# Performance work log

Hardware: AMD Instinct MI355X
Metric: run time of the kernel (lower is better)

## Reference

```python
import jax, jax.numpy as jnp
import numpy as np
from math import sqrt

BLOCK = 64  # block_size from init_kwargs


def setup_inputs() -> dict:
    key = jax.random.key(0)
    kq, kk, kv = jax.random.split(key, 3)
    b, t, e = 16, 8192, 64
    return {
        "Q": jax.random.normal(kq, (b, t, e), dtype=jnp.float32),
        "K": jax.random.normal(kk, (b, t, e), dtype=jnp.float32),
        "V": jax.random.normal(kv, (b, t, e), dtype=jnp.float32),
    }


def reference(Q, K, V):
    b, t, e = Q.shape
    # strided column indices: last position of every block
    cols = jnp.arange(BLOCK - 1, t, BLOCK)            # [n_cols] = [t // BLOCK]
    # scores of every query against the gathered key columns
    Z = jnp.einsum('bte,bce->btc', Q, K[:, cols]) / sqrt(e)  # [b, t, n_cols]
    # causal mask: query at position i may not attend to a column j > i
    causal = jnp.arange(t)[:, None] < cols[None, :]   # [t, n_cols], True = masked
    Z = jnp.where(causal, -jnp.inf, Z)
    # rows before the first column (i < BLOCK-1) are fully masked -> keep zeros
    A = jnp.zeros_like(Z).at[:, BLOCK - 1:].set(
        jax.nn.softmax(Z[:, BLOCK - 1:], axis=-1))
    out = jnp.einsum('btc,bce->bte', A, V[:, cols])   # [b, t, e]
    return out, A
```

## Files before the change

kernel.cpp:

```cpp
#include <hip/hip_runtime.h>
#include <math.h>


#define TSEQ 8192
#define EDIM 64
#define NCOL 128
#define NBATCH 16
#define MPG 4

typedef __attribute__((ext_vector_type(8))) short short8;
typedef __attribute__((ext_vector_type(4))) float f32x4;

__device__ __forceinline__ unsigned short f2bf(float f) {
    unsigned int u = __float_as_uint(f);
    return (unsigned short)((u + 0x7fffu + ((u >> 16) & 1u)) >> 16);
}

__global__ __launch_bounds__(256, 2)
void cba_kernel(const float* __restrict__ Q,
                const float* __restrict__ K,
                const float* __restrict__ V,
                float* __restrict__ Out,
                float* __restrict__ A)
{
    __shared__ unsigned short Kc[NCOL][72];
    __shared__ unsigned short VcT[EDIM][136];
    __shared__ unsigned short Aw[64][136];

    const int tid  = threadIdx.x;
    const int lane = tid & 63;
    const int wid  = tid >> 6;
    const int b    = blockIdx.x >> 5;
    const int mg   = blockIdx.x & 31;

    const int c   = lane & 15;
    const int kq  = (lane >> 4) << 3;
    const int rb  = (wid << 4) + ((lane >> 4) << 2);
    const int qr  = (wid << 4) + c;

    float4 qf[4];
    {
        const int m0 = mg * MPG;
        const float* qp = Q + ((size_t)b * TSEQ + (m0 << 6) + qr) * EDIM;
        qf[0] = *(const float4*)(qp + kq);
        qf[1] = *(const float4*)(qp + kq + 4);
        qf[2] = *(const float4*)(qp + 32 + kq);
        qf[3] = *(const float4*)(qp + 32 + kq + 4);
    }

    {
        const int j = tid >> 1;
        const int h = (tid & 1) << 5;
        const size_t src = ((size_t)b * TSEQ + (j * 64 + 63)) * EDIM + h;
        const float4* ks = (const float4*)(K + src);
        const float4* vs = (const float4*)(V + src);
        #pragma unroll
        for (int t = 0; t < 8; ++t) {
            float4 kf = ks[t];
            unsigned int p0 = (unsigned int)f2bf(kf.x) | ((unsigned int)f2bf(kf.y) << 16);
            unsigned int p1 = (unsigned int)f2bf(kf.z) | ((unsigned int)f2bf(kf.w) << 16);
            *(unsigned int*)&Kc[j][h + 4 * t]     = p0;
            *(unsigned int*)&Kc[j][h + 4 * t + 2] = p1;
        }
        #pragma unroll
        for (int t = 0; t < 8; ++t) {
            float4 vf = vs[t];
            VcT[h + 4 * t + 0][j] = f2bf(vf.x);
            VcT[h + 4 * t + 1][j] = f2bf(vf.y);
            VcT[h + 4 * t + 2][j] = f2bf(vf.z);
            VcT[h + 4 * t + 3][j] = f2bf(vf.w);
        }
    }
    __syncthreads();

    for (int it = 0; it < MPG; ++it) {
        const int m = mg * MPG + it;
        const size_t rowbase = (size_t)b * TSEQ + ((size_t)m << 6);

        short8 qa[2];
        #pragma unroll
        for (int s = 0; s < 2; ++s) {
            float4 f0 = qf[2 * s], f1 = qf[2 * s + 1];
            short8 v;
            v[0] = (short)f2bf(f0.x * 0.125f); v[1] = (short)f2bf(f0.y * 0.125f);
            v[2] = (short)f2bf(f0.z * 0.125f); v[3] = (short)f2bf(f0.w * 0.125f);
            v[4] = (short)f2bf(f1.x * 0.125f); v[5] = (short)f2bf(f1.y * 0.125f);
            v[6] = (short)f2bf(f1.z * 0.125f); v[7] = (short)f2bf(f1.w * 0.125f);
            qa[s] = v;
        }

        f32x4 acc[8];
        #pragma unroll
        for (int t = 0; t < 8; ++t) acc[t] = (f32x4)0.f;
        #pragma unroll
        for (int t = 0; t < 8; ++t) {
            const unsigned short* kr = &Kc[(t << 4) + c][0];
            short8 b0 = *(const short8*)(kr + kq);
            short8 b1 = *(const short8*)(kr + 32 + kq);
            acc[t] = __builtin_amdgcn_mfma_f32_16x16x32_bf16(qa[0], b0, acc[t], 0, 0, 0);
            acc[t] = __builtin_amdgcn_mfma_f32_16x16x32_bf16(qa[1], b1, acc[t], 0, 0, 0);
        }

        if (it + 1 < MPG) {
            const float* qp = Q + (rowbase + 64 + qr) * EDIM;
            qf[0] = *(const float4*)(qp + kq);
            qf[1] = *(const float4*)(qp + kq + 4);
            qf[2] = *(const float4*)(qp + 32 + kq);
            qf[3] = *(const float4*)(qp + 32 + kq + 4);
        }

        #pragma unroll
        for (int reg = 0; reg < 4; ++reg) {
            const int r  = rb + reg;
            const int nv = m + (r == 63 ? 1 : 0);
            float sum = 0.f;
            #pragma unroll
            for (int t = 0; t < 8; ++t) {
                const int jc = (t << 4) + c;
                float e = (jc < nv) ? __expf(acc[t][reg]) : 0.f;
                acc[t][reg] = e;
                sum += e;
            }
            sum += __shfl_xor(sum, 1); sum += __shfl_xor(sum, 2);
            sum += __shfl_xor(sum, 4); sum += __shfl_xor(sum, 8);
            const float rinv = (sum > 0.f) ? 1.0f / sum : 0.f;
            #pragma unroll
            for (int t = 0; t < 8; ++t) acc[t][reg] *= rinv;
        }

        #pragma unroll
        for (int reg = 0; reg < 4; ++reg) {
            float* ap = A + (rowbase + rb + reg) * NCOL + c;
            #pragma unroll
            for (int t = 0; t < 8; ++t) ap[t << 4] = acc[t][reg];
        }

        __syncthreads();

        #pragma unroll
        for (int reg = 0; reg < 4; ++reg) {
            #pragma unroll
            for (int t = 0; t < 8; ++t)
                Aw[rb + reg][(t << 4) + c] = f2bf(acc[t][reg]);
        }
        __syncthreads();

        short8 af[4];
        {
            const unsigned short* ar = &Aw[qr][0];
            #pragma unroll
            for (int s = 0; s < 4; ++s) af[s] = *(const short8*)(ar + (s << 5) + kq);
        }
        f32x4 oacc[4];
        #pragma unroll
        for (int t = 0; t < 4; ++t) oacc[t] = (f32x4)0.f;
        #pragma unroll
        for (int t = 0; t < 4; ++t) {
            const unsigned short* vr = &VcT[(t << 4) + c][0];
            #pragma unroll
            for (int s = 0; s < 4; ++s) {
                short8 vb = *(const short8*)(vr + (s << 5) + kq);
                oacc[t] = __builtin_amdgcn_mfma_f32_16x16x32_bf16(af[s], vb, oacc[t], 0, 0, 0);
            }
        }

        #pragma unroll
        for (int t = 0; t < 4; ++t) {
            #pragma unroll
            for (int reg = 0; reg < 4; ++reg)
                Out[(rowbase + rb + reg) * EDIM + (t << 4) + c] = oacc[t][reg];
        }
    }
}

extern "C" void kernel_launch(void* const* d_in, const int* in_sizes, int n_in,
                              void* d_out, int out_size, void* d_ws, size_t ws_size,
                              hipStream_t stream) {
    const float* Q = (const float*)d_in[0];
    const float* K = (const float*)d_in[1];
    const float* V = (const float*)d_in[2];
    float* Out = (float*)d_out;
    float* A   = Out + (size_t)NBATCH * TSEQ * EDIM;

    cba_kernel<<<dim3(NBATCH * 32), dim3(256), 0, stream>>>(Q, K, V, Out, A);
}
```

Baseline: 171.9 us.

## Transpose MFMA operands so each lane owns a row, vectorize stores, drop barriers

Swaps the A/B operands of both MFMA stages so the accumulator is transposed: each lane now holds four consecutive columns of a single query row. Row-softmax sums then need only two cross-lane shuffles, and the A and Out writes become 16-byte vector stores instead of scalar strided stores. Each wave writes and reads only its own 16 rows of the shared Aw tile, so the two block-wide __syncthreads are replaced by a compiler barrier and an LDS waitcnt. The risk is correctness if the wave-local LDS ordering assumption fails, plus more LDS bank conflicts on the short4 writes.

```diff
diff --git a/kernel.cpp b/kernel.cpp
--- a/kernel.cpp
+++ b/kernel.cpp
@@ -9,6 +9,7 @@
 #define MPG 4
 
 typedef __attribute__((ext_vector_type(8))) short short8;
+typedef __attribute__((ext_vector_type(4))) short short4v;
 typedef __attribute__((ext_vector_type(4))) float f32x4;
 
 __device__ __forceinline__ unsigned short f2bf(float f) {
@@ -34,14 +35,15 @@
     const int mg   = blockIdx.x & 31;
 
     const int c   = lane & 15;
-    const int kq  = (lane >> 4) << 3;
-    const int rb  = (wid << 4) + ((lane >> 4) << 2);
-    const int qr  = (wid << 4) + c;
+    const int g   = lane >> 4;
+    const int kq  = g << 3;
+    const int cb  = g << 2;
+    const int r   = (wid << 4) + c;
 
     float4 qf[4];
     {
         const int m0 = mg * MPG;
-        const float* qp = Q + ((size_t)b * TSEQ + (m0 << 6) + qr) * EDIM;
+        const float* qp = Q + ((size_t)b * TSEQ + (m0 << 6) + r) * EDIM;
         qf[0] = *(const float4*)(qp + kq);
         qf[1] = *(const float4*)(qp + kq + 4);
         qf[2] = *(const float4*)(qp + 32 + kq);
@@ -97,78 +99,81 @@
             const unsigned short* kr = &Kc[(t << 4) + c][0];
             short8 b0 = *(const short8*)(kr + kq);
             short8 b1 = *(const short8*)(kr + 32 + kq);
-            acc[t] = __builtin_amdgcn_mfma_f32_16x16x32_bf16(qa[0], b0, acc[t], 0, 0, 0);
-            acc[t] = __builtin_amdgcn_mfma_f32_16x16x32_bf16(qa[1], b1, acc[t], 0, 0, 0);
+            acc[t] = __builtin_amdgcn_mfma_f32_16x16x32_bf16(b0, qa[0], acc[t], 0, 0, 0);
+            acc[t] = __builtin_amdgcn_mfma_f32_16x16x32_bf16(b1, qa[1], acc[t], 0, 0, 0);
         }
 
         if (it + 1 < MPG) {
-            const float* qp = Q + (rowbase + 64 + qr) * EDIM;
+            const float* qp = Q + (rowbase + 64 + r) * EDIM;
             qf[0] = *(const float4*)(qp + kq);
             qf[1] = *(const float4*)(qp + kq + 4);
             qf[2] = *(const float4*)(qp + 32 + kq);
             qf[3] = *(const float4*)(qp + 32 + kq + 4);
         }
 
+        const int nv = m + (r == 63 ? 1 : 0);
+        float sum = 0.f;
         #pragma unroll
-        for (int reg = 0; reg < 4; ++reg) {
-            const int r  = rb + reg;
-            const int nv = m + (r == 63 ? 1 : 0);
-            float sum = 0.f;
+        for (int t = 0; t < 8; ++t) {
+            const int j0 = (t << 4) + cb;
             #pragma unroll
-            for (int t = 0; t < 8; ++t) {
-                const int jc = (t << 4) + c;
-                float e = (jc < nv) ? __expf(acc[t][reg]) : 0.f;
+            for (int reg = 0; reg < 4; ++reg) {
+                float e = (j0 + reg < nv) ? __expf(acc[t][reg]) : 0.f;
                 acc[t][reg] = e;
                 sum += e;
             }
-            sum += __shfl_xor(sum, 1); sum += __shfl_xor(sum, 2);
-            sum += __shfl_xor(sum, 4); sum += __shfl_xor(sum, 8);
-            const float rinv = (sum > 0.f) ? 1.0f / sum : 0.f;
-            #pragma unroll
-            for (int t = 0; t < 8; ++t) acc[t][reg] *= rinv;
+        }
+        sum += __shfl_xor(sum, 16);
+        sum += __shfl_xor(sum, 32);
+        const float rinv = (sum > 0.f) ? 1.0f / sum : 0.f;
+        #pragma unroll
+        for (int t = 0; t < 8; ++t) {
+            acc[t][0] *= rinv; acc[t][1] *= rinv;
+            acc[t][2] *= rinv; acc[t][3] *= rinv;
         }
 
-        #pragma unroll
-        for (int reg = 0; reg < 4; ++reg) {
-            float* ap = A + (rowbase + rb + reg) * NCOL + c;
+        {
+            float* ap = A + (rowbase + r) * NCOL + cb;
             #pragma unroll
-            for (int t = 0; t < 8; ++t) ap[t << 4] = acc[t][reg];
+            for (int t = 0; t < 8; ++t)
+                *(f32x4*)(ap + (t << 4)) = acc[t];
         }
 
-        __syncthreads();
-
+        asm volatile("" ::: "memory");
         #pragma unroll
-        for (int reg = 0; reg < 4; ++reg) {
-            #pragma unroll
-            for (int t = 0; t < 8; ++t)
-                Aw[rb + reg][(t << 4) + c] = f2bf(acc[t][reg]);
+        for (int t = 0; t < 8; ++t) {
+            short4v w;
+            w[0] = (short)f2bf(acc[t][0]); w[1] = (short)f2bf(acc[t][1]);
+            w[2] = (short)f2bf(acc[t][2]); w[3] = (short)f2bf(acc[t][3]);
+            *(short4v*)&Aw[r][(t << 4) + cb] = w;
         }
-        __syncthreads();
+        asm volatile("s_waitcnt lgkmcnt(0)" ::: "memory");
 
         short8 af[4];
         {
-            const unsigned short* ar = &Aw[qr][0];
+            const unsigned short* ar = &Aw[r][0];
             #pragma unroll
-            for (int s = 0; s < 4; ++s) af[s] = *(const short8*)(ar + (s << 5) + kq);
+            for (int s = 0; s < 4; ++s)
+                af[s] = *(const short8*)(ar + (s << 5) + kq);
         }
         f32x4 oacc[4];
         #pragma unroll
-        for (int t = 0; t < 4; ++t) oacc[t] = (f32x4)0.f;
+        for (int te = 0; te < 4; ++te) oacc[te] = (f32x4)0.f;
         #pragma unroll
-        for (int t = 0; t < 4; ++t) {
-            const unsigned short* vr = &VcT[(t << 4) + c][0];
+        for (int te = 0; te < 4; ++te) {
+            const unsigned short* vr = &VcT[(te << 4) + c][0];
             #pragma unroll
             for (int s = 0; s < 4; ++s) {
-                short8 vb = *(const short8*)(vr + (s << 5) + kq);
-                oacc[t] = __builtin_amdgcn_mfma_f32_16x16x32_bf16(af[s], vb, oacc[t], 0, 0, 0);
+                short8 va = *(const short8*)(vr + (s << 5) + kq);
+                oacc[te] = __builtin_amdgcn_mfma_f32_16x16x32_bf16(va, af[s], oacc[te], 0, 0, 0);
             }
         }
 
-        #pragma unroll
-        for (int t = 0; t < 4; ++t) {
+        {
+            float* op = Out + (rowbase + r) * EDIM + cb;
             #pragma unroll
-            for (int reg = 0; reg < 4; ++reg)
-                Out[(rowbase + rb + reg) * EDIM + (t << 4) + c] = oacc[t][reg];
+            for (int te = 0; te < 4; ++te)
+                *(f32x4*)(op + (te << 4)) = oacc[te];
         }
     }
 }
```

Result: no change. 174.8 us (+1.7%).
